# Performance work log

Measured on AMD Instinct MI355X. Metric: run time of the kernel, lower is better.

Reference implementation:

```python
import jax, jax.numpy as jnp
import numpy as np

A_LO = 0      # interval lower bound
B_HI = 63     # interval upper bound -> window W = 64
PAD_BIG = 1.0e4  # finite pad so exp(-scale*PAD_BIG) == 0 exactly in fp32 (no inf/nan grads)


def setup_inputs() -> dict:
    key = jax.random.key(0)
    k1, k2 = jax.random.split(key)
    B, T = 64, 2048
    phi = jax.random.normal(k1, (B, T, 2), dtype=jnp.float32)
    psi = jax.random.normal(k2, (B, T, 2), dtype=jnp.float32)
    return {"phi": phi, "psi": psi, "scale": 8}


def reference(phi, psi, scale):
    # phi, psi: [B, T, 2] robustness traces of left/right subformulas.
    a, b = A_LO, B_HI
    Bsz, T, _ = phi.shape
    W = b - a + 1
    s = jnp.float32(scale)

    # Pad time axis so every window of length W fits. phi padded with a large
    # value (neutral for smooth-min), psi with a large negative value (neutral
    # for smooth-max); both exactly neutral in fp32 since exp(-s*1e4) == 0.
    phi_pad = jnp.pad(phi, ((0, 0), (0, b), (0, 0)), constant_values=PAD_BIG)
    psi_pad = jnp.pad(psi, ((0, 0), (0, b), (0, 0)), constant_values=-PAD_BIG)

    # tau = t + a + j, j in [0, W)
    idx = jnp.arange(T)[:, None] + jnp.arange(a, b + 1)[None, :]  # [T, W]
    phi_win = phi_pad[:, idx]  # [B, T, W, 2], phi at t+k
    psi_win = psi_pad[:, idx]  # [B, T, W, 2], psi at tau

    # Smooth min over phi[t : tau] (exclusive of tau):
    #   min_phi(k) = -logsumexp_{s'=t..t+k-1}(-s*phi[s']) / s
    # computed via a cumulative logsumexp over the window axis.
    neg = -s * phi_win
    cumlse = jax.lax.associative_scan(jnp.logaddexp, neg, axis=2)  # [B,T,W,2]
    shifted = jnp.concatenate(
        [jnp.zeros_like(cumlse[:, :, :1]), cumlse[:, :, :-1]], axis=2)
    k_off = jnp.arange(W)[None, None, :, None] + a  # tau - t
    # tau == t -> min over empty segment -> ones (per original code)
    min_phi = jnp.where(k_off == 0, jnp.float32(1.0), -shifted / s)

    # Smooth min of the pair {min_phi, psi[tau]}
    cand = -jnp.logaddexp(-s * min_phi, -s * psi_win) / s  # [B,T,W,2]

    # Mask tau > T-1 (candidates that don't exist in the original loop).
    valid = (jnp.arange(T)[:, None] + a + jnp.arange(W)[None, :]) <= (T - 1)
    cand = jnp.where(valid[None, :, :, None], cand, -PAD_BIG)

    # Smooth max over candidate taus
    best = jax.nn.logsumexp(s * cand, axis=2) / s  # [B, T, 2]
    return best
```

## Files before the change

kernel.cpp:

```cpp
#include <hip/hip_runtime.h>


#define T_DIM   2048
#define W_WIN   64
#define BLOCK_T 256

__global__ __launch_bounds__(BLOCK_T) void until_kernel(
    const float* __restrict__ phi,
    const float* __restrict__ psi,
    const int*  __restrict__ scale_p,
    float* __restrict__ out)
{
    __shared__ float2 s_phi[BLOCK_T + W_WIN - 1];
    __shared__ float2 s_psi[BLOCK_T + W_WIN - 1];

    const int b   = blockIdx.y;
    const int t0  = blockIdx.x * BLOCK_T;
    const int tid = threadIdx.x;
    const float s = (float)(*scale_p);

    const float2* __restrict__ phi2 = (const float2*)(phi + (size_t)b * T_DIM * 2);
    const float2* __restrict__ psi2 = (const float2*)(psi + (size_t)b * T_DIM * 2);

    for (int i = tid; i < BLOCK_T + W_WIN - 1; i += BLOCK_T) {
        int t = t0 + i;
        float2 pv = make_float2(0.f, 0.f);
        float2 qv = make_float2(0.f, 0.f);
        if (t < T_DIM) { pv = phi2[t]; qv = psi2[t]; }
        s_phi[i] = pv;
        s_psi[i] = qv;
    }
    __syncthreads();

    const int t = t0 + tid;
    const int K = min(W_WIN, T_DIM - t);
    const float Es = __expf(-s);

    float2 q0 = s_psi[tid];
    float acc0 = __builtin_amdgcn_rcpf(Es + __expf(-s * q0.x));
    float acc1 = __builtin_amdgcn_rcpf(Es + __expf(-s * q0.y));
    float2 p0 = s_phi[tid];
    float sum0 = __expf(-s * p0.x);
    float sum1 = __expf(-s * p0.y);

    #pragma unroll 7
    for (int k = 1; k < K; ++k) {
        float2 pp = s_phi[tid + k];
        float2 qq = s_psi[tid + k];
        acc0 += __builtin_amdgcn_rcpf(sum0 + __expf(-s * qq.x));
        acc1 += __builtin_amdgcn_rcpf(sum1 + __expf(-s * qq.y));
        sum0 += __expf(-s * pp.x);
        sum1 += __expf(-s * pp.y);
    }

    float2* __restrict__ out2 = (float2*)(out + (size_t)b * T_DIM * 2);
    out2[t] = make_float2(__logf(acc0) / s, __logf(acc1) / s);
}

extern "C" void kernel_launch(void* const* d_in, const int* in_sizes, int n_in,
                              void* d_out, int out_size, void* d_ws, size_t ws_size,
                              hipStream_t stream) {
    const float* phi   = (const float*)d_in[0];
    const float* psi   = (const float*)d_in[1];
    const int*   scale = (const int*)d_in[2];
    float* out = (float*)d_out;

    const int B = in_sizes[0] / (T_DIM * 2);
    dim3 grid(T_DIM / BLOCK_T, B);
    until_kernel<<<grid, dim3(BLOCK_T), 0, stream>>>(phi, psi, scale, out);
}
```

Measured before the change: 64.48 us.

## Precompute exponentials once per element in shared staging and fully unroll window loop

Each staged element's exp(-s*phi) and exp(-s*psi) is now computed once while loading into a single float4 shared buffer, so the inner loop no longer recomputes four exponentials per window step. Out-of-range positions are padded with 0 and +inf, which replaces the per-thread variable trip count with a fixed, fully unrolled 64-step loop. The accumulator is split into two chains to shorten dependency latency. In exchange it relies on rcp(inf)=0 for padding and uses wider shared loads.

```diff
diff --git a/kernel.cpp b/kernel.cpp
--- a/kernel.cpp
+++ b/kernel.cpp
@@ -1,9 +1,11 @@
 #include <hip/hip_runtime.h>
+#include <math.h>
 
 
 #define T_DIM   2048
 #define W_WIN   64
 #define BLOCK_T 256
+#define STAGE   (BLOCK_T + W_WIN - 1)
 
 __global__ __launch_bounds__(BLOCK_T) void until_kernel(
     const float* __restrict__ phi,
@@ -11,50 +13,58 @@
     const int*  __restrict__ scale_p,
     float* __restrict__ out)
 {
-    __shared__ float2 s_phi[BLOCK_T + W_WIN - 1];
-    __shared__ float2 s_psi[BLOCK_T + W_WIN - 1];
+    __shared__ float4 s_d[STAGE];
 
     const int b   = blockIdx.y;
     const int t0  = blockIdx.x * BLOCK_T;
     const int tid = threadIdx.x;
-    const float s = (float)(*scale_p);
+    const float s  = (float)(*scale_p);
+    const float ns = -s;
 
     const float2* __restrict__ phi2 = (const float2*)(phi + (size_t)b * T_DIM * 2);
     const float2* __restrict__ psi2 = (const float2*)(psi + (size_t)b * T_DIM * 2);
 
-    for (int i = tid; i < BLOCK_T + W_WIN - 1; i += BLOCK_T) {
+    for (int i = tid; i < STAGE; i += BLOCK_T) {
         int t = t0 + i;
-        float2 pv = make_float2(0.f, 0.f);
-        float2 qv = make_float2(0.f, 0.f);
-        if (t < T_DIM) { pv = phi2[t]; qv = psi2[t]; }
-        s_phi[i] = pv;
-        s_psi[i] = qv;
+        float4 v;
+        if (t < T_DIM) {
+            float2 pv = phi2[t];
+            float2 qv = psi2[t];
+            v.x = __expf(ns * pv.x);
+            v.y = __expf(ns * pv.y);
+            v.z = __expf(ns * qv.x);
+            v.w = __expf(ns * qv.y);
+        } else {
+            v.x = 0.f; v.y = 0.f;
+            v.z = INFINITY; v.w = INFINITY;
+        }
+        s_d[i] = v;
     }
     __syncthreads();
 
-    const int t = t0 + tid;
-    const int K = min(W_WIN, T_DIM - t);
-    const float Es = __expf(-s);
+    const float Es = __expf(ns);
 
-    float2 q0 = s_psi[tid];
-    float acc0 = __builtin_amdgcn_rcpf(Es + __expf(-s * q0.x));
-    float acc1 = __builtin_amdgcn_rcpf(Es + __expf(-s * q0.y));
-    float2 p0 = s_phi[tid];
-    float sum0 = __expf(-s * p0.x);
-    float sum1 = __expf(-s * p0.y);
+    float4 v0 = s_d[tid];
+    float accA0 = __builtin_amdgcn_rcpf(Es + v0.z);
+    float accA1 = __builtin_amdgcn_rcpf(Es + v0.w);
+    float accB0 = 0.f, accB1 = 0.f;
+    float sum0 = v0.x;
+    float sum1 = v0.y;
 
-    #pragma unroll 7
-    for (int k = 1; k < K; ++k) {
-        float2 pp = s_phi[tid + k];
-        float2 qq = s_psi[tid + k];
-        acc0 += __builtin_amdgcn_rcpf(sum0 + __expf(-s * qq.x));
-        acc1 += __builtin_amdgcn_rcpf(sum1 + __expf(-s * qq.y));
-        sum0 += __expf(-s * pp.x);
-        sum1 += __expf(-s * pp.y);
+    #pragma unroll
+    for (int k = 1; k < W_WIN; ++k) {
+        float4 v = s_d[tid + k];
+        float r0 = __builtin_amdgcn_rcpf(sum0 + v.z);
+        float r1 = __builtin_amdgcn_rcpf(sum1 + v.w);
+        if (k & 1) { accA0 += r0; accA1 += r1; }
+        else       { accB0 += r0; accB1 += r1; }
+        sum0 += v.x;
+        sum1 += v.y;
     }
 
+    const int t = t0 + tid;
     float2* __restrict__ out2 = (float2*)(out + (size_t)b * T_DIM * 2);
-    out2[t] = make_float2(__logf(acc0) / s, __logf(acc1) / s);
+    out2[t] = make_float2(__logf(accA0 + accB0) / s, __logf(accA1 + accB1) / s);
 }
 
 extern "C" void kernel_launch(void* const* d_in, const int* in_sizes, int n_in,
```

Measured after the change: 61.46 us. 4.7% less time.
